# Kernel tuning notes

Measured on AMD Instinct MI355X. Metric: run time of the kernel, lower is better.

The kernel has to match this reference:

```python
import jax, jax.numpy as jnp
import numpy as np

B, S, H, NH = 2, 2048, 1024, 16
HD = H // NH  # head size = 64


def setup_inputs() -> dict:
    key = jax.random.key(0)
    ks = jax.random.split(key, 6)
    x = jax.random.normal(ks[0], (B, S, H), dtype=jnp.float32)
    additive_attention_mask = jnp.zeros((S,), dtype=jnp.float32)
    # nn.Linear params: weight [out, in], bias [out]
    w_qkv = jax.random.normal(ks[1], (3 * H, H), dtype=jnp.float32) / np.sqrt(H)
    b_qkv = jax.random.normal(ks[2], (3 * H,), dtype=jnp.float32) * 0.02
    w_o = jax.random.normal(ks[3], (H, H), dtype=jnp.float32) / np.sqrt(H)
    b_o = jax.random.normal(ks[4], (H,), dtype=jnp.float32) * 0.02
    return {"x": x, "additive_attention_mask": additive_attention_mask,
            "w_qkv": w_qkv, "b_qkv": b_qkv, "w_o": w_o, "b_o": b_o}


def reference(x, additive_attention_mask, w_qkv, b_qkv, w_o, b_o):
    # QKV projection: (B,S,H) @ (H,3H) + (3H,)
    qkv = jnp.einsum('bsh,oh->bso', x, w_qkv) + b_qkv
    q, k, v = qkv[..., :H], qkv[..., H:2 * H], qkv[..., 2 * H:]
    # split heads -> (B, NH, S, HD)
    def heads(t):
        return t.reshape(B, S, NH, HD).transpose(0, 2, 1, 3)
    qh, kh, vh = heads(q), heads(k), heads(v)
    # scores (B, NH, Sq, Sk); mask added BEFORE the 1/sqrt(d) scaling (faithful)
    scores = jnp.einsum('bhqd,bhkd->bhqk', qh, kh)
    scores = scores + additive_attention_mask[None, None, None, :]
    probs = jax.nn.softmax(scores / np.sqrt(HD).astype(np.float32), axis=-1)
    # dropout p=0.0 -> identity
    av = jnp.einsum('bhqk,bhkd->bqhd', probs, vh).reshape(B, S, H)
    return jnp.einsum('bsh,oh->bso', av, w_o) + b_o
```

## Files before the change

### kernel.cpp

```cpp
#include <hip/hip_runtime.h>
#include <cmath>

#define B_  2
#define S_  2048
#define H_  1024
#define NH_ 16
#define HD_ 64

typedef _Float16 half8  __attribute__((ext_vector_type(8)));
typedef __fp16   fp16x2 __attribute__((ext_vector_type(2)));
typedef float    f32x16 __attribute__((ext_vector_type(16)));

#define MFMA32(a, b, c) __builtin_amdgcn_mfma_f32_32x32x16_f16((a), (b), (c), 0, 0, 0)

__device__ __forceinline__ void gl2lds16(const void* g, void* l) {
    __builtin_amdgcn_global_load_lds(
        (const __attribute__((address_space(1))) unsigned int*)g,
        (__attribute__((address_space(3))) unsigned int*)l,
        16, 0, 0);
}

__device__ __forceinline__ unsigned pk16(float a, float b) {
    union { fp16x2 v; unsigned u; } c;
    c.v = __builtin_amdgcn_cvt_pkrtz(a, b);
    return c.u;
}

__device__ __forceinline__ float exp2_hw(float x) {
#if __has_builtin(__builtin_amdgcn_exp2f)
    return __builtin_amdgcn_exp2f(x);
#else
    return __expf(x * 0.6931471805599453f);
#endif
}

#define LOG2E   1.4426950408889634f
#define SCALE_  (0.125f * LOG2E)
#define THR2_   11.5415603f

__global__ __launch_bounds__(256, 4)
void conv_hilo(const float* __restrict__ src, _Float16* __restrict__ dh,
               _Float16* __restrict__ dl, int K)
{
    const int bid = blockIdx.x;
    const int nkt = K >> 6;
    const int rt  = bid / nkt;
    const int kt  = bid % nkt;
    const int tid = threadIdx.x;
    const size_t tb = (size_t)bid * 8192;
#pragma unroll
    for (int p = 0; p < 4; ++p) {
        const int idx = p * 256 + tid;
        const int r   = idx >> 3;
        const int g   = idx & 7;
        const float* s = src + (size_t)(rt * 128 + r) * K + kt * 64 + g * 8;
        const float4 v0 = *reinterpret_cast<const float4*>(s);
        const float4 v1 = *reinterpret_cast<const float4*>(s + 4);
        const float f[8] = {v0.x, v0.y, v0.z, v0.w, v1.x, v1.y, v1.z, v1.w};
        half8 hi, lo;
#pragma unroll
        for (int e = 0; e < 8; ++e) {
            const _Float16 hv = (_Float16)f[e];
            hi[e] = hv;
            lo[e] = (_Float16)(f[e] - (float)hv);
        }
        const int dst = r * 64 + ((g ^ (r & 7)) << 3);
        *reinterpret_cast<half8*>(dh + tb + dst) = hi;
        *reinterpret_cast<half8*>(dl + tb + dst) = lo;
    }
}

template<int QKV>
__global__ __launch_bounds__(256, 1)
void hgemm_split(const _Float16* __restrict__ Ah, const _Float16* __restrict__ Al,
                 const _Float16* __restrict__ Wh, const _Float16* __restrict__ Wl,
                 const float* __restrict__ bias, float* __restrict__ C,
                 float* __restrict__ Qo,
                 _Float16* __restrict__ Kh, _Float16* __restrict__ Kl,
                 _Float16* __restrict__ Vh, _Float16* __restrict__ Vl,
                 int nbm, int nbn, int nkt, int N)
{
    __shared__ __align__(16) unsigned char smem[131072];

    const int tid  = threadIdx.x;
    const int w    = tid >> 6;
    const int lane = tid & 63;
    const int lr   = lane & 31;
    const int hh   = lane >> 5;
    const int wm   = w >> 1, wn = w & 1;

    const int nwg = nbm * nbn;
    const int cpx = nwg >> 3;
    const int bid = blockIdx.x;
    const int wg  = (bid & 7) * cpx + (bid >> 3);
    const int mt  = wg / nbn, nt = wg % nbn;

    const size_t aBase = (size_t)mt * nkt * 8192;
    const size_t wBase = (size_t)nt * nkt * 8192;

    f32x16 acc[2][2];
#pragma unroll
    for (int mi = 0; mi < 2; ++mi)
#pragma unroll
        for (int ni = 0; ni < 2; ++ni)
#pragma unroll
            for (int r = 0; r < 16; ++r) acc[mi][ni][r] = 0.f;

    auto stage = [&](int kt, int buf) {
        const size_t at = aBase + (size_t)kt * 8192;
        const size_t wt = wBase + (size_t)kt * 8192;
        unsigned char* sb = smem + (buf << 16);
#pragma unroll
        for (int c = 0; c < 4; ++c) {
            const int loff = (w * 4 + c) * 512;
            const int goff = loff + lane * 8;
            gl2lds16((const void*)(Ah + at + goff), (void*)((_Float16*)sb + loff));
            gl2lds16((const void*)(Al + at + goff), (void*)((_Float16*)(sb + 16384) + loff));
            gl2lds16((const void*)(Wh + wt + goff), (void*)((_Float16*)(sb + 32768) + loff));
            gl2lds16((const void*)(Wl + wt + goff), (void*)((_Float16*)(sb + 49152) + loff));
        }
    };

    stage(0, 0);
    __syncthreads();

    for (int kt = 0; kt < nkt; ++kt) {
        if (kt + 1 < nkt) stage(kt + 1, (kt + 1) & 1);

        unsigned char* sb = smem + ((kt & 1) << 16);
        _Float16* sAh = (_Float16*)(sb);
        _Float16* sAl = (_Float16*)(sb + 16384);
        _Float16* sWh = (_Float16*)(sb + 32768);
        _Float16* sWl = (_Float16*)(sb + 49152);

#pragma unroll
        for (int ks = 0; ks < 4; ++ks) {
            const int g = ks * 2 + hh;
            half8 aH[2], aL[2], bH[2], bL[2];
#pragma unroll
            for (int mi = 0; mi < 2; ++mi) {
                const int r   = wm * 64 + mi * 32 + lr;
                const int idx = r * 64 + ((g ^ (r & 7)) << 3);
                aH[mi] = *reinterpret_cast<const half8*>(sAh + idx);
                aL[mi] = *reinterpret_cast<const half8*>(sAl + idx);
            }
#pragma unroll
            for (int ni = 0; ni < 2; ++ni) {
                const int c   = wn * 64 + ni * 32 + lr;
                const int idx = c * 64 + ((g ^ (c & 7)) << 3);
                bH[ni] = *reinterpret_cast<const half8*>(sWh + idx);
                bL[ni] = *reinterpret_cast<const half8*>(sWl + idx);
            }
#pragma unroll
            for (int mi = 0; mi < 2; ++mi)
#pragma unroll
                for (int ni = 0; ni < 2; ++ni) {
                    acc[mi][ni] = MFMA32(aH[mi], bH[ni], acc[mi][ni]);
                    acc[mi][ni] = MFMA32(aH[mi], bL[ni], acc[mi][ni]);
                    acc[mi][ni] = MFMA32(aL[mi], bH[ni], acc[mi][ni]);
                }
        }
        __syncthreads();
    }

    if constexpr (QKV == 0) {
        const int n0 = nt * 128 + wn * 64 + lr;
        float bv[2];
#pragma unroll
        for (int ni = 0; ni < 2; ++ni) bv[ni] = bias[n0 + ni * 32];
#pragma unroll
        for (int mi = 0; mi < 2; ++mi)
#pragma unroll
            for (int ni = 0; ni < 2; ++ni)
#pragma unroll
                for (int r = 0; r < 16; ++r) {
                    const int m = mt * 128 + wm * 64 + mi * 32 +
                                  (r & 3) + 8 * (r >> 2) + 4 * hh;
                    C[(size_t)m * N + n0 + ni * 32] = acc[mi][ni][r] + bv[ni];
                }
    } else {
        float* sC = (float*)smem;
        const int m0  = mt * 128;
        const int b   = m0 >> 11;
        const int kt0 = (m0 & 2047) >> 6;
#pragma unroll
        for (int pass = 0; pass < 2; ++pass) {
            __syncthreads();
            if (wm == pass) {
#pragma unroll
                for (int mi = 0; mi < 2; ++mi)
#pragma unroll
                    for (int ni = 0; ni < 2; ++ni)
#pragma unroll
                        for (int r = 0; r < 16; ++r) {
                            const int ml = mi * 32 + (r & 3) + 8 * (r >> 2) + 4 * hh;
                            sC[ml * 132 + wn * 64 + ni * 32 + lr] = acc[mi][ni][r];
                        }
            }
            __syncthreads();
            const int ktile = kt0 + pass;
            if (nt < 8) {
#pragma unroll
                for (int it = 0; it < 8; ++it) {
                    const int idx = it * 256 + tid;
                    const int row = idx >> 5;
                    const int c4  = (idx & 31) << 2;
                    float4 v = *reinterpret_cast<const float4*>(&sC[row * 132 + c4]);
                    const float4 bv = *reinterpret_cast<const float4*>(bias + nt * 128 + c4);
                    v.x += bv.x; v.y += bv.y; v.z += bv.z; v.w += bv.w;
                    *reinterpret_cast<float4*>(
                        Qo + (size_t)(m0 + pass * 64 + row) * 1024 + nt * 128 + c4) = v;
                }
            } else if (nt < 16) {
#pragma unroll
                for (int it = 0; it < 4; ++it) {
                    const int idx = it * 256 + tid;
                    const int key = idx >> 4;
                    const int g   = idx & 15;
                    const int head = 2 * (nt - 8) + (g >> 3);
                    const int d0   = (g & 7) << 3;
                    float f[8];
#pragma unroll
                    for (int e = 0; e < 8; ++e)
                        f[e] = sC[key * 132 + g * 8 + e] +
                               bias[1024 + (nt - 8) * 128 + g * 8 + e];
                    half8 hi, lo;
#pragma unroll
                    for (int e = 0; e < 8; ++e) {
                        const _Float16 hv = (_Float16)f[e];
                        hi[e] = hv;
                        lo[e] = (_Float16)(f[e] - (float)hv);
                    }
                    const size_t base = ((size_t)(b * 16 + head) * 32 + ktile) * 4096;
                    const size_t dst  = base + key * 64 + (d0 ^ ((key & 7) << 3));
                    *reinterpret_cast<half8*>(Kh + dst) = hi;
                    *reinterpret_cast<half8*>(Kl + dst) = lo;
                }
            } else {
#pragma unroll
                for (int it = 0; it < 4; ++it) {
                    const int idx = it * 256 + tid;
                    const int f   = idx >> 3;
                    const int kg  = idx & 7;
                    const int head = 2 * (nt - 16) + (f >> 6);
                    const int d    = f & 63;
                    const float bv = bias[2048 + (nt - 16) * 128 + f];
                    float fe[8];
#pragma unroll
                    for (int e = 0; e < 8; ++e)
                        fe[e] = sC[(kg * 8 + e) * 132 + f] + bv;
                    half8 hi, lo;
#pragma unroll
                    for (int e = 0; e < 8; ++e) {
                        const _Float16 hv = (_Float16)fe[e];
                        hi[e] = hv;
                        lo[e] = (_Float16)(fe[e] - (float)hv);
                    }
                    const size_t base = ((size_t)(b * 16 + head) * 32 + ktile) * 4096;
                    const size_t dst  = base + d * 64 + ((kg * 8) ^ ((d & 7) << 3));
                    *reinterpret_cast<half8*>(Vh + dst) = hi;
                    *reinterpret_cast<half8*>(Vl + dst) = lo;
                }
            }
        }
    }
}

__global__ __launch_bounds__(256, 2)
void attn_mfma(const float* __restrict__ Q, const float* __restrict__ mask,
               const _Float16* __restrict__ Kh, const _Float16* __restrict__ Kl,
               const _Float16* __restrict__ Vh, const _Float16* __restrict__ Vl,
               _Float16* __restrict__ Avh, _Float16* __restrict__ Avl)
{
    __shared__ __align__(16) unsigned char smem[73728];
    float* sM = (float*)(smem + 65536);
    float* sO = (float*)(smem);

    const int tid  = threadIdx.x;
    const int w    = tid >> 6;
    const int lane = tid & 63;
    const int lq   = lane & 31;
    const int hh   = lane >> 5;

    const int bid = blockIdx.x;
    const int wg  = (bid & 7) * 64 + (bid >> 3);
    const int bh  = wg >> 4;
    const int qb  = wg & 15;
    const int b   = bh >> 4, h = bh & 15;

    {
        const float4* mg = reinterpret_cast<const float4*>(mask);
        float4* ms = reinterpret_cast<float4*>(sM);
        float4 a = mg[tid], c = mg[tid + 256];
        a.x *= SCALE_; a.y *= SCALE_; a.z *= SCALE_; a.w *= SCALE_;
        c.x *= SCALE_; c.y *= SCALE_; c.z *= SCALE_; c.w *= SCALE_;
        ms[tid] = a; ms[tid + 256] = c;
    }

    const int qrow = b * S_ + qb * 128 + w * 32 + lq;
    half8 qh[4], ql[4];
#pragma unroll
    for (int ks = 0; ks < 4; ++ks) {
        const float* qp = Q + (size_t)qrow * 1024 + h * HD_ + ks * 16 + hh * 8;
        const float4 a = *reinterpret_cast<const float4*>(qp);
        const float4 c = *reinterpret_cast<const float4*>(qp + 4);
        float qf[8] = {a.x, a.y, a.z, a.w, c.x, c.y, c.z, c.w};
#pragma unroll
        for (int e = 0; e < 8; ++e) {
            const float sv = qf[e] * SCALE_;
            const _Float16 hv = (_Float16)sv;
            qh[ks][e] = hv;
            ql[ks][e] = (_Float16)(sv - (float)hv);
        }
    }

    const int swz = (lq & 7) << 3;
    int off[2][4];
#pragma unroll
    for (int t2 = 0; t2 < 2; ++t2)
#pragma unroll
        for (int ks = 0; ks < 4; ++ks)
            off[t2][ks] = (t2 * 32 + lq) * 64 + ((ks * 16 + hh * 8) ^ swz);

    f32x16 o0 = {0,0,0,0,0,0,0,0,0,0,0,0,0,0,0,0};
    f32x16 o1 = {0,0,0,0,0,0,0,0,0,0,0,0,0,0,0,0};
    float m_run = -INFINITY, l_run = 0.f;

    const size_t bhbase = (size_t)bh * 32 * 4096;

    {
        const size_t tb = bhbase;
#pragma unroll
        for (int i = 0; i < 2; ++i) {
            const int loff = (w * 2 + i) * 512;
            const int goff = loff + lane * 8;
            _Float16* nb = (_Float16*)smem;
            gl2lds16((const void*)(Kh + tb + goff), (void*)(nb + loff));
            gl2lds16((const void*)(Kl + tb + goff), (void*)(nb + 4096 + loff));
            gl2lds16((const void*)(Vh + tb + goff), (void*)(nb + 8192 + loff));
            gl2lds16((const void*)(Vl + tb + goff), (void*)(nb + 12288 + loff));
        }
    }
    __syncthreads();

    for (int kt = 0; kt < 32; ++kt) {
        _Float16* bb = (_Float16*)(smem + ((kt & 1) << 15));
        if (kt < 31) {
            _Float16* nb = (_Float16*)(smem + (((kt + 1) & 1) << 15));
            const size_t tb = bhbase + (size_t)(kt + 1) * 4096;
#pragma unroll
            for (int i = 0; i < 2; ++i) {
                const int loff = (w * 2 + i) * 512;
                const int goff = loff + lane * 8;
                gl2lds16((const void*)(Kh + tb + goff), (void*)(nb + loff));
                gl2lds16((const void*)(Kl + tb + goff), (void*)(nb + 4096 + loff));
                gl2lds16((const void*)(Vh + tb + goff), (void*)(nb + 8192 + loff));
                gl2lds16((const void*)(Vl + tb + goff), (void*)(nb + 12288 + loff));
            }
        }

        f32x16 st[2];
#pragma unroll
        for (int ktt = 0; ktt < 2; ++ktt) {
            f32x16 acc = {0,0,0,0,0,0,0,0,0,0,0,0,0,0,0,0};
#pragma unroll
            for (int ks = 0; ks < 4; ++ks) {
                const half8 ka = *reinterpret_cast<const half8*>(bb + off[ktt][ks]);
                const half8 kb = *reinterpret_cast<const half8*>(bb + 4096 + off[ktt][ks]);
                acc = MFMA32(ka, qh[ks], acc);
                acc = MFMA32(ka, ql[ks], acc);
                acc = MFMA32(kb, qh[ks], acc);
            }
            st[ktt] = acc;
        }

        float mx = -INFINITY;
#pragma unroll
        for (int ktt = 0; ktt < 2; ++ktt) {
#pragma unroll
            for (int rr = 0; rr < 4; ++rr) {
                const int key0 = kt * 64 + ktt * 32 + rr * 8 + hh * 4;
                const float4 mk = *reinterpret_cast<const float4*>(sM + key0);
                const float mkv[4] = {mk.x, mk.y, mk.z, mk.w};
#pragma unroll
                for (int c = 0; c < 4; ++c) {
                    const int r = rr * 4 + c;
                    const float tv = st[ktt][r] + mkv[c];
                    st[ktt][r] = tv;
                    mx = fmaxf(mx, tv);
                }
            }
        }
        mx = fmaxf(mx, __shfl_xor(mx, 32));

        if (!__all(mx - m_run <= THR2_)) {
            const float mnew = fmaxf(m_run, mx);
            const float corr = exp2_hw(m_run - mnew);
            m_run = mnew;
            l_run *= corr;
#pragma unroll
            for (int r = 0; r < 16; ++r) { o0[r] *= corr; o1[r] *= corr; }
        }
        float ps = 0.f;
#pragma unroll
        for (int ktt = 0; ktt < 2; ++ktt)
#pragma unroll
            for (int r = 0; r < 16; ++r) {
                const float p = exp2_hw(st[ktt][r] - m_run);
                st[ktt][r] = p;
                ps += p;
            }
        ps += __shfl_xor(ps, 32);
        l_run += ps;

        unsigned wph[2][4][2], wpl[2][4][2];
#pragma unroll
        for (int ktt = 0; ktt < 2; ++ktt)
#pragma unroll
            for (int rr = 0; rr < 4; ++rr)
#pragma unroll
                for (int pp = 0; pp < 2; ++pp) {
                    const float p0 = st[ktt][rr * 4 + pp * 2 + 0];
                    const float p1 = st[ktt][rr * 4 + pp * 2 + 1];
                    union { fp16x2 v; unsigned u; } hw;
                    hw.v = __builtin_amdgcn_cvt_pkrtz(p0, p1);
                    wph[ktt][rr][pp] = hw.u;
                    wpl[ktt][rr][pp] = pk16(p0 - (float)hw.v[0], p1 - (float)hw.v[1]);
                }

#pragma unroll
        for (int ks = 0; ks < 4; ++ks) {
            const int i1 = ks >> 1;
            const int rA = (ks & 1) * 2;
            union { unsigned u[4]; half8 v; } ph, pl;
            {
                const unsigned oA0 = wph[i1][rA + 0][0], oB0 = wph[i1][rA + 0][1];
                const unsigned oA1 = wph[i1][rA + 1][0], oB1 = wph[i1][rA + 1][1];
                const unsigned sA1 = (unsigned)__shfl_xor((int)oA1, 32);
                const unsigned sB1 = (unsigned)__shfl_xor((int)oB1, 32);
                const unsigned sA0 = (unsigned)__shfl_xor((int)oA0, 32);
                const unsigned sB0 = (unsigned)__shfl_xor((int)oB0, 32);
                ph.u[0] = hh ? sA1 : oA0;
                ph.u[1] = hh ? sB1 : oB0;
                ph.u[2] = hh ? oA1 : sA0;
                ph.u[3] = hh ? oB1 : sB0;
            }
            {
                const unsigned oA0 = wpl[i1][rA + 0][0], oB0 = wpl[i1][rA + 0][1];
                const unsigned oA1 = wpl[i1][rA + 1][0], oB1 = wpl[i1][rA + 1][1];
                const unsigned sA1 = (unsigned)__shfl_xor((int)oA1, 32);
                const unsigned sB1 = (unsigned)__shfl_xor((int)oB1, 32);
                const unsigned sA0 = (unsigned)__shfl_xor((int)oA0, 32);
                const unsigned sB0 = (unsigned)__shfl_xor((int)oB0, 32);
                pl.u[0] = hh ? sA1 : oA0;
                pl.u[1] = hh ? sB1 : oB0;
                pl.u[2] = hh ? oA1 : sA0;
                pl.u[3] = hh ? oB1 : sB0;
            }
#pragma unroll
            for (int dt = 0; dt < 2; ++dt) {
                const half8 va = *reinterpret_cast<const half8*>(bb + 8192 + off[dt][ks]);
                const half8 vb = *reinterpret_cast<const half8*>(bb + 12288 + off[dt][ks]);
                if (dt == 0) {
                    o0 = MFMA32(va, ph.v, o0);
                    o0 = MFMA32(va, pl.v, o0);
                    o0 = MFMA32(vb, ph.v, o0);
                } else {
                    o1 = MFMA32(va, ph.v, o1);
                    o1 = MFMA32(va, pl.v, o1);
                    o1 = MFMA32(vb, ph.v, o1);
                }
            }
        }
        __syncthreads();
    }

    const float inv = 1.f / l_run;
#pragma unroll
    for (int dt = 0; dt < 2; ++dt)
#pragma unroll
        for (int r = 0; r < 16; ++r) {
            const int d = dt * 32 + (r & 3) + 8 * (r >> 2) + 4 * hh;
            sO[(w * 32 + lq) * 68 + d] = (dt ? o1[r] : o0[r]) * inv;
        }
    __syncthreads();
    {
        const size_t tb = (((size_t)(b * 16 + qb)) * 16 + h) * 8192;
#pragma unroll
        for (int p = 0; p < 4; ++p) {
            const int idx = p * 256 + tid;
            const int q = idx >> 3, g = idx & 7;
            const float4 v0 = *reinterpret_cast<const float4*>(&sO[q * 68 + g * 8]);
            const float4 v1 = *reinterpret_cast<const float4*>(&sO[q * 68 + g * 8 + 4]);
            const float f[8] = {v0.x, v0.y, v0.z, v0.w, v1.x, v1.y, v1.z, v1.w};
            half8 hi, lo;
#pragma unroll
            for (int e = 0; e < 8; ++e) {
                const _Float16 hv = (_Float16)f[e];
                hi[e] = hv;
                lo[e] = (_Float16)(f[e] - (float)hv);
            }
            const int dst = q * 64 + ((g ^ (q & 7)) << 3);
            *reinterpret_cast<half8*>(Avh + tb + dst) = hi;
            *reinterpret_cast<half8*>(Avl + tb + dst) = lo;
        }
    }
}

extern "C" void kernel_launch(void* const* d_in, const int* in_sizes, int n_in,
                              void* d_out, int out_size, void* d_ws, size_t ws_size,
                              hipStream_t stream)
{
    const float* x     = (const float*)d_in[0];
    const float* mask  = (const float*)d_in[1];
    const float* w_qkv = (const float*)d_in[2];
    const float* b_qkv = (const float*)d_in[3];
    const float* w_o   = (const float*)d_in[4];
    const float* b_o   = (const float*)d_in[5];
    float* out = (float*)d_out;

    char* p = (char*)d_ws;
    float*    Qarr = (float*)p;             p += (size_t)4096 * 1024 * 4;
    _Float16* Kh   = (_Float16*)p;          p += (size_t)32 * 32 * 4096 * 2;
    _Float16* Kl   = (_Float16*)p;          p += (size_t)32 * 32 * 4096 * 2;
    _Float16* Vh   = (_Float16*)p;          p += (size_t)32 * 32 * 4096 * 2;
    _Float16* Vl   = (_Float16*)p;          p += (size_t)32 * 32 * 4096 * 2;
    _Float16* Xh   = (_Float16*)p;          p += (size_t)4096 * 1024 * 2;
    _Float16* Xl   = (_Float16*)p;          p += (size_t)4096 * 1024 * 2;
    _Float16* Wqh  = (_Float16*)p;          p += (size_t)3072 * 1024 * 2;
    _Float16* Wql  = (_Float16*)p;          p += (size_t)3072 * 1024 * 2;
    _Float16* Woh  = (_Float16*)p;          p += (size_t)1024 * 1024 * 2;
    _Float16* Wol  = (_Float16*)p;          p += (size_t)1024 * 1024 * 2;
    _Float16* Avh  = (_Float16*)p;          p += (size_t)4096 * 1024 * 2;
    _Float16* Avl  = (_Float16*)p;          p += (size_t)4096 * 1024 * 2;

    const dim3 blk(256);
    conv_hilo<<<dim3(32 * 16), blk, 0, stream>>>(x,     Xh,  Xl,  1024);
    conv_hilo<<<dim3(24 * 16), blk, 0, stream>>>(w_qkv, Wqh, Wql, 1024);
    conv_hilo<<<dim3(8 * 16),  blk, 0, stream>>>(w_o,   Woh, Wol, 1024);

    hgemm_split<1><<<dim3(32 * 24), blk, 0, stream>>>(
        Xh, Xl, Wqh, Wql, b_qkv, nullptr, Qarr, Kh, Kl, Vh, Vl, 32, 24, 16, 3072);
    attn_mfma<<<dim3(512), blk, 0, stream>>>(Qarr, mask, Kh, Kl, Vh, Vl, Avh, Avl);
    hgemm_split<0><<<dim3(32 * 8), blk, 0, stream>>>(
        Avh, Avl, Woh, Wol, b_o, out, nullptr, nullptr, nullptr, nullptr, nullptr,
        32, 8, 16, 1024);
}
```

Measured before the change: 335.3 us.

## Halve GEMM K-tile for two blocks per CU, add setprio, drop P low-part MFMA

The GEMM K-tile shrinks from 64 to 32. That halves LDS use to 64KB, so two blocks can run per CU (launch bounds 256,2), and the conversion kernels and the attention output layout change to a 32-wide tiled swizzle to match. s_setprio wraps the MFMA clusters in both the GEMM and attention kernels so the math waves get issue priority. In the attention PV product the low-precision correction term for P is dropped, removing a third of those MFMAs and the related shuffles. The cost is lower accuracy in the probabilities and a K loop with twice as many iterations.

```diff
diff --git a/kernel.cpp b/kernel.cpp
--- a/kernel.cpp
+++ b/kernel.cpp
@@ -38,22 +38,24 @@
 #define SCALE_  (0.125f * LOG2E)
 #define THR2_   11.5415603f
 
+#define GSWZ(r, g) (((g) ^ (((r) >> 1) & 3)) << 3)
+
 __global__ __launch_bounds__(256, 4)
 void conv_hilo(const float* __restrict__ src, _Float16* __restrict__ dh,
                _Float16* __restrict__ dl, int K)
 {
     const int bid = blockIdx.x;
-    const int nkt = K >> 6;
+    const int nkt = K >> 5;
     const int rt  = bid / nkt;
-    const int kt  = bid % nkt;
+    const int ktc = bid % nkt;
     const int tid = threadIdx.x;
-    const size_t tb = (size_t)bid * 8192;
-#pragma unroll
-    for (int p = 0; p < 4; ++p) {
+    const size_t tb = (size_t)bid * 4096;
+#pragma unroll
+    for (int p = 0; p < 2; ++p) {
         const int idx = p * 256 + tid;
-        const int r   = idx >> 3;
-        const int g   = idx & 7;
-        const float* s = src + (size_t)(rt * 128 + r) * K + kt * 64 + g * 8;
+        const int r   = idx >> 2;
+        const int g   = idx & 3;
+        const float* s = src + (size_t)(rt * 128 + r) * K + ktc * 32 + g * 8;
         const float4 v0 = *reinterpret_cast<const float4*>(s);
         const float4 v1 = *reinterpret_cast<const float4*>(s + 4);
         const float f[8] = {v0.x, v0.y, v0.z, v0.w, v1.x, v1.y, v1.z, v1.w};
@@ -64,14 +66,14 @@
             hi[e] = hv;
             lo[e] = (_Float16)(f[e] - (float)hv);
         }
-        const int dst = r * 64 + ((g ^ (r & 7)) << 3);
+        const int dst = r * 32 + GSWZ(r, g);
         *reinterpret_cast<half8*>(dh + tb + dst) = hi;
         *reinterpret_cast<half8*>(dl + tb + dst) = lo;
     }
 }
 
 template<int QKV>
-__global__ __launch_bounds__(256, 1)
+__global__ __launch_bounds__(256, 2)
 void hgemm_split(const _Float16* __restrict__ Ah, const _Float16* __restrict__ Al,
                  const _Float16* __restrict__ Wh, const _Float16* __restrict__ Wl,
                  const float* __restrict__ bias, float* __restrict__ C,
@@ -80,14 +82,15 @@
                  _Float16* __restrict__ Vh, _Float16* __restrict__ Vl,
                  int nbm, int nbn, int nkt, int N)
 {
-    __shared__ __align__(16) unsigned char smem[131072];
+    __shared__ __align__(16) unsigned char smem[65536];
 
     const int tid  = threadIdx.x;
     const int w    = tid >> 6;
     const int lane = tid & 63;
     const int lr   = lane & 31;
     const int hh   = lane >> 5;
-    const int wm   = w >> 1, wn = w & 1;
+    const int wm   = w >> 1;
+    const int wn   = w & 1;
 
     const int nwg = nbm * nbn;
     const int cpx = nwg >> 3;
@@ -95,8 +98,8 @@
     const int wg  = (bid & 7) * cpx + (bid >> 3);
     const int mt  = wg / nbn, nt = wg % nbn;
 
-    const size_t aBase = (size_t)mt * nkt * 8192;
-    const size_t wBase = (size_t)nt * nkt * 8192;
+    const size_t aBase = (size_t)mt * nkt * 4096;
+    const size_t wBase = (size_t)nt * nkt * 4096;
 
     f32x16 acc[2][2];
 #pragma unroll
@@ -107,17 +110,16 @@
             for (int r = 0; r < 16; ++r) acc[mi][ni][r] = 0.f;
 
     auto stage = [&](int kt, int buf) {
-        const size_t at = aBase + (size_t)kt * 8192;
-        const size_t wt = wBase + (size_t)kt * 8192;
-        unsigned char* sb = smem + (buf << 16);
-#pragma unroll
-        for (int c = 0; c < 4; ++c) {
-            const int loff = (w * 4 + c) * 512;
-            const int goff = loff + lane * 8;
-            gl2lds16((const void*)(Ah + at + goff), (void*)((_Float16*)sb + loff));
-            gl2lds16((const void*)(Al + at + goff), (void*)((_Float16*)(sb + 16384) + loff));
-            gl2lds16((const void*)(Wh + wt + goff), (void*)((_Float16*)(sb + 32768) + loff));
-            gl2lds16((const void*)(Wl + wt + goff), (void*)((_Float16*)(sb + 49152) + loff));
+        const size_t at = aBase + (size_t)kt * 4096;
+        const size_t wt = wBase + (size_t)kt * 4096;
+        unsigned char* sb = smem + (buf << 15);
+#pragma unroll
+        for (int c = 0; c < 2; ++c) {
+            const int off = (c * 256 + tid) * 8;
+            gl2lds16((const void*)(Ah + at + off), (void*)((_Float16*)sb + off));
+            gl2lds16((const void*)(Al + at + off), (void*)((_Float16*)(sb + 8192) + off));
+            gl2lds16((const void*)(Wh + wt + off), (void*)((_Float16*)(sb + 16384) + off));
+            gl2lds16((const void*)(Wl + wt + off), (void*)((_Float16*)(sb + 24576) + off));
         }
     };
 
@@ -127,30 +129,31 @@
     for (int kt = 0; kt < nkt; ++kt) {
         if (kt + 1 < nkt) stage(kt + 1, (kt + 1) & 1);
 
-        unsigned char* sb = smem + ((kt & 1) << 16);
+        unsigned char* sb = smem + ((kt & 1) << 15);
         _Float16* sAh = (_Float16*)(sb);
-        _Float16* sAl = (_Float16*)(sb + 16384);
-        _Float16* sWh = (_Float16*)(sb + 32768);
-        _Float16* sWl = (_Float16*)(sb + 49152);
-
-#pragma unroll
-        for (int ks = 0; ks < 4; ++ks) {
+        _Float16* sAl = (_Float16*)(sb + 8192);
+        _Float16* sWh = (_Float16*)(sb + 16384);
+        _Float16* sWl = (_Float16*)(sb + 24576);
+
+#pragma unroll
+        for (int ks = 0; ks < 2; ++ks) {
             const int g = ks * 2 + hh;
             half8 aH[2], aL[2], bH[2], bL[2];
 #pragma unroll
             for (int mi = 0; mi < 2; ++mi) {
                 const int r   = wm * 64 + mi * 32 + lr;
-                const int idx = r * 64 + ((g ^ (r & 7)) << 3);
+                const int idx = r * 32 + GSWZ(r, g);
                 aH[mi] = *reinterpret_cast<const half8*>(sAh + idx);
                 aL[mi] = *reinterpret_cast<const half8*>(sAl + idx);
             }
 #pragma unroll
             for (int ni = 0; ni < 2; ++ni) {
                 const int c   = wn * 64 + ni * 32 + lr;
-                const int idx = c * 64 + ((g ^ (c & 7)) << 3);
+                const int idx = c * 32 + GSWZ(c, g);
                 bH[ni] = *reinterpret_cast<const half8*>(sWh + idx);
                 bL[ni] = *reinterpret_cast<const half8*>(sWl + idx);
             }
+            __builtin_amdgcn_s_setprio(1);
 #pragma unroll
             for (int mi = 0; mi < 2; ++mi)
 #pragma unroll
@@ -159,6 +162,7 @@
                     acc[mi][ni] = MFMA32(aH[mi], bL[ni], acc[mi][ni]);
                     acc[mi][ni] = MFMA32(aL[mi], bH[ni], acc[mi][ni]);
                 }
+            __builtin_amdgcn_s_setprio(0);
         }
         __syncthreads();
     }
@@ -363,6 +367,7 @@
 #pragma unroll
         for (int ktt = 0; ktt < 2; ++ktt) {
             f32x16 acc = {0,0,0,0,0,0,0,0,0,0,0,0,0,0,0,0};
+            __builtin_amdgcn_s_setprio(1);
 #pragma unroll
             for (int ks = 0; ks < 4; ++ks) {
                 const half8 ka = *reinterpret_cast<const half8*>(bb + off[ktt][ks]);
@@ -371,6 +376,7 @@
                 acc = MFMA32(ka, ql[ks], acc);
                 acc = MFMA32(kb, qh[ks], acc);
             }
+            __builtin_amdgcn_s_setprio(0);
             st[ktt] = acc;
         }
 
@@ -413,26 +419,21 @@
         ps += __shfl_xor(ps, 32);
         l_run += ps;
 
-        unsigned wph[2][4][2], wpl[2][4][2];
+        unsigned wph[2][4][2];
 #pragma unroll
         for (int ktt = 0; ktt < 2; ++ktt)
 #pragma unroll
             for (int rr = 0; rr < 4; ++rr)
 #pragma unroll
-                for (int pp = 0; pp < 2; ++pp) {
-                    const float p0 = st[ktt][rr * 4 + pp * 2 + 0];
-                    const float p1 = st[ktt][rr * 4 + pp * 2 + 1];
-                    union { fp16x2 v; unsigned u; } hw;
-                    hw.v = __builtin_amdgcn_cvt_pkrtz(p0, p1);
-                    wph[ktt][rr][pp] = hw.u;
-                    wpl[ktt][rr][pp] = pk16(p0 - (float)hw.v[0], p1 - (float)hw.v[1]);
-                }
+                for (int pp = 0; pp < 2; ++pp)
+                    wph[ktt][rr][pp] = pk16(st[ktt][rr * 4 + pp * 2 + 0],
+                                            st[ktt][rr * 4 + pp * 2 + 1]);
 
 #pragma unroll
         for (int ks = 0; ks < 4; ++ks) {
             const int i1 = ks >> 1;
             const int rA = (ks & 1) * 2;
-            union { unsigned u[4]; half8 v; } ph, pl;
+            union { unsigned u[4]; half8 v; } ph;
             {
                 const unsigned oA0 = wph[i1][rA + 0][0], oB0 = wph[i1][rA + 0][1];
                 const unsigned oA1 = wph[i1][rA + 1][0], oB1 = wph[i1][rA + 1][1];
@@ -445,32 +446,20 @@
                 ph.u[2] = hh ? oA1 : sA0;
                 ph.u[3] = hh ? oB1 : sB0;
             }
-            {
-                const unsigned oA0 = wpl[i1][rA + 0][0], oB0 = wpl[i1][rA + 0][1];
-                const unsigned oA1 = wpl[i1][rA + 1][0], oB1 = wpl[i1][rA + 1][1];
-                const unsigned sA1 = (unsigned)__shfl_xor((int)oA1, 32);
-                const unsigned sB1 = (unsigned)__shfl_xor((int)oB1, 32);
-                const unsigned sA0 = (unsigned)__shfl_xor((int)oA0, 32);
-                const unsigned sB0 = (unsigned)__shfl_xor((int)oB0, 32);
-                pl.u[0] = hh ? sA1 : oA0;
-                pl.u[1] = hh ? sB1 : oB0;
-                pl.u[2] = hh ? oA1 : sA0;
-                pl.u[3] = hh ? oB1 : sB0;
-            }
+            __builtin_amdgcn_s_setprio(1);
 #pragma unroll
             for (int dt = 0; dt < 2; ++dt) {
                 const half8 va = *reinterpret_cast<const half8*>(bb + 8192 + off[dt][ks]);
                 const half8 vb = *reinterpret_cast<const half8*>(bb + 12288 + off[dt][ks]);
                 if (dt == 0) {
                     o0 = MFMA32(va, ph.v, o0);
-                    o0 = MFMA32(va, pl.v, o0);
                     o0 = MFMA32(vb, ph.v, o0);
                 } else {
                     o1 = MFMA32(va, ph.v, o1);
-                    o1 = MFMA32(va, pl.v, o1);
                     o1 = MFMA32(vb, ph.v, o1);
                 }
             }
+            __builtin_amdgcn_s_setprio(0);
         }
         __syncthreads();
     }
@@ -485,7 +474,7 @@
         }
     __syncthreads();
     {
-        const size_t tb = (((size_t)(b * 16 + qb)) * 16 + h) * 8192;
+        const size_t tbase = (((size_t)(b * 16 + qb)) * 32 + h * 2) * 4096;
 #pragma unroll
         for (int p = 0; p < 4; ++p) {
             const int idx = p * 256 + tid;
@@ -500,9 +489,10 @@
                 hi[e] = hv;
                 lo[e] = (_Float16)(f[e] - (float)hv);
             }
-            const int dst = q * 64 + ((g ^ (q & 7)) << 3);
-            *reinterpret_cast<half8*>(Avh + tb + dst) = hi;
-            *reinterpret_cast<half8*>(Avl + tb + dst) = lo;
+            const int th = g >> 2, g2 = g & 3;
+            const size_t dst = tbase + th * 4096 + q * 32 + GSWZ(q, g2);
+            *reinterpret_cast<half8*>(Avh + dst) = hi;
+            *reinterpret_cast<half8*>(Avl + dst) = lo;
         }
     }
 }
@@ -534,15 +524,14 @@
     _Float16* Avh  = (_Float16*)p;          p += (size_t)4096 * 1024 * 2;
     _Float16* Avl  = (_Float16*)p;          p += (size_t)4096 * 1024 * 2;
 
-    const dim3 blk(256);
-    conv_hilo<<<dim3(32 * 16), blk, 0, stream>>>(x,     Xh,  Xl,  1024);
-    conv_hilo<<<dim3(24 * 16), blk, 0, stream>>>(w_qkv, Wqh, Wql, 1024);
-    conv_hilo<<<dim3(8 * 16),  blk, 0, stream>>>(w_o,   Woh, Wol, 1024);
-
-    hgemm_split<1><<<dim3(32 * 24), blk, 0, stream>>>(
-        Xh, Xl, Wqh, Wql, b_qkv, nullptr, Qarr, Kh, Kl, Vh, Vl, 32, 24, 16, 3072);
-    attn_mfma<<<dim3(512), blk, 0, stream>>>(Qarr, mask, Kh, Kl, Vh, Vl, Avh, Avl);
-    hgemm_split<0><<<dim3(32 * 8), blk, 0, stream>>>(
+    conv_hilo<<<dim3(32 * 32), dim3(256), 0, stream>>>(x,     Xh,  Xl,  1024);
+    conv_hilo<<<dim3(24 * 32), dim3(256), 0, stream>>>(w_qkv, Wqh, Wql, 1024);
+    conv_hilo<<<dim3(8 * 32),  dim3(256), 0, stream>>>(w_o,   Woh, Wol, 1024);
+
+    hgemm_split<1><<<dim3(32 * 24), dim3(256), 0, stream>>>(
+        Xh, Xl, Wqh, Wql, b_qkv, nullptr, Qarr, Kh, Kl, Vh, Vl, 32, 24, 32, 3072);
+    attn_mfma<<<dim3(512), dim3(256), 0, stream>>>(Qarr, mask, Kh, Kl, Vh, Vl, Avh, Avl);
+    hgemm_split<0><<<dim3(32 * 8), dim3(256), 0, stream>>>(
         Avh, Avl, Woh, Wol, b_o, out, nullptr, nullptr, nullptr, nullptr, nullptr,
-        32, 8, 16, 1024);
-}
+        32, 8, 32, 1024);
+}
```

Result: faster. 300.8 us (-10.3%).
